# Kernel optimization log

Measured on AMD Instinct MI355X. Metric: run time of the kernel, lower is better.

The kernel has to match this reference:

```python
import jax, jax.numpy as jnp
import numpy as np

N_NODES = 8192
N_UND = 65536      # undirected pairs placed
N_DIR = 131072     # extra directed edges placed


def _build_graph():
    rng = np.random.default_rng(0)
    A = np.zeros((N_NODES, N_NODES), np.float32)
    # undirected pairs (i<j), both directions set
    ii = rng.integers(0, N_NODES, 4 * N_UND)
    jj = rng.integers(0, N_NODES, 4 * N_UND)
    m = ii < jj
    iu, ju = ii[m][:N_UND], jj[m][:N_UND]
    A[iu, ju] = 1.0
    A[ju, iu] = 1.0
    # extra directed edges
    di = rng.integers(0, N_NODES, 2 * N_DIR)
    dj = rng.integers(0, N_NODES, 2 * N_DIR)
    m2 = di != dj
    A[di[m2][:N_DIR], dj[m2][:N_DIR]] = 1.0
    # dense_to_sparse: row, col of nonzeros
    row, col = np.nonzero(A)
    edge_index = np.stack([row, col]).astype(np.int32)
    # undirected mask: A==1 & A.T==1, upper triangle
    und = np.triu((A == 1.0) & (A.T == 1.0))
    u, v = np.nonzero(und)
    undirected_edges = np.stack([u, v], axis=1).astype(np.int32)
    return A, edge_index, undirected_edges


def setup_inputs() -> dict:
    key = jax.random.key(0)
    ks = jax.random.split(key, 4)
    A, edge_index, undirected_edges = _build_graph()
    N = N_NODES
    return {
        "adjacency": jnp.asarray(A),
        "W1": jax.random.normal(ks[0], (N, 16), jnp.float32) * 0.05,
        "b1": jnp.zeros((16,), jnp.float32),
        "W2": jax.random.normal(ks[1], (16, 8), jnp.float32) * 0.25,
        "b2": jnp.zeros((8,), jnp.float32),
        "Wfc": jax.random.normal(ks[2], (16, 1), jnp.float32) * 0.25,
        "bfc": jnp.zeros((1,), jnp.float32),
        "edge_index": jnp.asarray(edge_index),
        "undirected_edges": jnp.asarray(undirected_edges),
    }


def reference(adjacency, W1, b1, W2, b2, Wfc, bfc, edge_index, undirected_edges):
    N = adjacency.shape[0]
    src, dst = edge_index[0], edge_index[1]
    E = src.shape[0]
    # GCN normalization with self-loops (PyG gcn_norm): deg over target nodes
    deg = jax.ops.segment_sum(jnp.ones((E,), adjacency.dtype), dst,
                              num_segments=N) + 1.0
    dinv = jax.lax.rsqrt(deg)                       # deg >= 1, no inf
    norm = dinv[src] * dinv[dst]                    # [E]
    self_w = (dinv * dinv)[:, None]                 # self-loop coeff [N,1]

    def conv(h):  # h: [N, F] -> normalized scatter-add aggregation
        msg = norm[:, None] * h[src]                # [E, F]
        return jax.ops.segment_sum(msg, dst, num_segments=N) + self_w * h

    # node_features = eye(N), so eye(N) @ W1 == W1
    x = jax.nn.relu(conv(W1) + b1)                  # [N, 16]
    x = jax.nn.relu(conv(x @ W2) + b2)              # [N, 8]

    u, v = undirected_edges[:, 0], undirected_edges[:, 1]
    ef = jnp.concatenate([x[u], x[v]], axis=1)      # [U, 16]
    orient = jax.nn.sigmoid(ef @ Wfc + bfc)[:, 0]   # [U]

    out = adjacency.at[u, v].set(orient).at[v, u].set(1.0 - orient)
    return out
```

## Files before the change

kernel.cpp:

```cpp
#include <hip/hip_runtime.h>
#include <math.h>

#define F1 16
#define F2 8

__global__ void k_edges0(const int* __restrict__ src, const int* __restrict__ dst,
                         float* __restrict__ out, float* __restrict__ deg,
                         int E, int N) {
    int e = blockIdx.x * blockDim.x + threadIdx.x;
    if (e < E) {
        int s = src[e], d = dst[e];
        out[(long)s * N + d] = 1.0f;
        atomicAdd(&deg[d], 1.0f);
    }
}

__global__ void k_conv1_edges(const int* __restrict__ src, const int* __restrict__ dst,
                              const float* __restrict__ deg, const float* __restrict__ W1,
                              float* __restrict__ x1, int E) {
    int id = blockIdx.x * blockDim.x + threadIdx.x;
    int e = id >> 4;
    int f = id & (F1 - 1);
    if (e < E) {
        int s = src[e], d = dst[e];
        float nrm = rsqrtf((deg[s] + 1.0f) * (deg[d] + 1.0f));
        atomicAdd(&x1[(long)d * F1 + f], nrm * W1[(long)s * F1 + f]);
    }
}

__global__ void k_layer1(const float* __restrict__ deg, const float* __restrict__ b1,
                         const float* __restrict__ W1, const float* __restrict__ W2,
                         const float* __restrict__ x1, float* __restrict__ h2, int N) {
    int id = blockIdx.x * blockDim.x + threadIdx.x;
    if (id < N * F2) {
        int i = id >> 3;
        int g = id & (F2 - 1);
        float sw = 1.0f / (deg[i] + 1.0f);
        float acc = 0.0f;
        #pragma unroll
        for (int f = 0; f < F1; ++f) {
            float v = x1[(long)i * F1 + f] + sw * W1[(long)i * F1 + f] + b1[f];
            v = v > 0.0f ? v : 0.0f;
            acc += v * W2[f * F2 + g];
        }
        h2[(long)i * F2 + g] = acc;
    }
}

__global__ void k_conv2_edges(const int* __restrict__ src, const int* __restrict__ dst,
                              const float* __restrict__ deg, const float* __restrict__ h2,
                              float* __restrict__ x2, int E) {
    int id = blockIdx.x * blockDim.x + threadIdx.x;
    int e = id >> 3;
    int g = id & (F2 - 1);
    if (e < E) {
        int s = src[e], d = dst[e];
        float nrm = rsqrtf((deg[s] + 1.0f) * (deg[d] + 1.0f));
        atomicAdd(&x2[(long)d * F2 + g], nrm * h2[(long)s * F2 + g]);
    }
}

__global__ void k_orient(const int2* __restrict__ ue, const float* __restrict__ x2,
                         const float* __restrict__ h2, const float* __restrict__ deg,
                         const float* __restrict__ b2, const float* __restrict__ Wfc,
                         const float* __restrict__ bfc, float* __restrict__ out,
                         int U, int N) {
    int k = blockIdx.x * blockDim.x + threadIdx.x;
    if (k < U) {
        int2 e = ue[k];
        int u = e.x, v = e.y;
        float swu = 1.0f / (deg[u] + 1.0f);
        float swv = 1.0f / (deg[v] + 1.0f);
        float s = bfc[0];
        #pragma unroll
        for (int g = 0; g < F2; ++g) {
            float xu = x2[(long)u * F2 + g] + swu * h2[(long)u * F2 + g] + b2[g];
            float xv = x2[(long)v * F2 + g] + swv * h2[(long)v * F2 + g] + b2[g];
            xu = xu > 0.0f ? xu : 0.0f;
            xv = xv > 0.0f ? xv : 0.0f;
            s += xu * Wfc[g] + xv * Wfc[F2 + g];
        }
        float orient = 1.0f / (1.0f + expf(-s));
        out[(long)u * N + v] = orient;
        out[(long)v * N + u] = 1.0f - orient;
    }
}

extern "C" void kernel_launch(void* const* d_in, const int* in_sizes, int n_in,
                              void* d_out, int out_size, void* d_ws, size_t ws_size,
                              hipStream_t stream) {
    const float* W1  = (const float*)d_in[1];
    const float* b1  = (const float*)d_in[2];
    const float* W2  = (const float*)d_in[3];
    const float* b2  = (const float*)d_in[4];
    const float* Wfc = (const float*)d_in[5];
    const float* bfc = (const float*)d_in[6];
    const int* edge_index = (const int*)d_in[7];
    const int2* und       = (const int2*)d_in[8];

    int N = in_sizes[1] / F1;
    int E = in_sizes[7] / 2;
    int U = in_sizes[8] / 2;
    const int* src = edge_index;
    const int* dst = edge_index + E;

    float* ws  = (float*)d_ws;
    float* deg = ws;
    float* x1  = ws + N;
    float* x2  = x1 + (long)F1 * N;
    float* h2  = x2 + (long)F2 * N;

    const int B = 256;

    hipMemsetAsync(d_out, 0, (size_t)N * N * sizeof(float), stream);
    hipMemsetAsync(d_ws, 0, (size_t)(N + (long)F1 * N + (long)F2 * N) * sizeof(float), stream);

    k_edges0<<<(E + B - 1) / B, B, 0, stream>>>(src, dst, (float*)d_out, deg, E, N);

    {
        long work = (long)E * F1;
        k_conv1_edges<<<(int)((work + B - 1) / B), B, 0, stream>>>(src, dst, deg, W1, x1, E);
    }
    k_layer1<<<(N * F2 + B - 1) / B, B, 0, stream>>>(deg, b1, W1, W2, x1, h2, N);

    {
        long work = (long)E * F2;
        k_conv2_edges<<<(int)((work + B - 1) / B), B, 0, stream>>>(src, dst, deg, h2, x2, E);
    }

    k_orient<<<(U + B - 1) / B, B, 0, stream>>>(und, x2, h2, deg, b2, Wfc, bfc,
                                                (float*)d_out, U, N);
}
```

Before: 448.6 us.

## Overlap output zero-fill with GCN stages and write edge ones last

The separate 256 MB memset of the dense output is removed. Its zeroing is split into three chunks, each handled by extra blocks added to the conv1, layer1 and conv2 kernels, so the bandwidth-bound fill runs alongside the small atomic-heavy graph kernels. Setting the 1.0 edge entries moves into the final orientation kernel, which now reads the input adjacency to skip reverse-present pairs, because those entries are overwritten by orientation values. This adds reads of the adjacency and makes the fill depend on the extra blocks being scheduled well.

```diff
diff --git a/kernel.cpp b/kernel.cpp
--- a/kernel.cpp
+++ b/kernel.cpp
@@ -4,67 +4,87 @@
 #define F1 16
 #define F2 8
 
-__global__ void k_edges0(const int* __restrict__ src, const int* __restrict__ dst,
-                         float* __restrict__ out, float* __restrict__ deg,
-                         int E, int N) {
+__global__ void k_deg(const int* __restrict__ dst, float* __restrict__ deg, int E) {
     int e = blockIdx.x * blockDim.x + threadIdx.x;
-    if (e < E) {
-        int s = src[e], d = dst[e];
-        out[(long)s * N + d] = 1.0f;
-        atomicAdd(&deg[d], 1.0f);
+    if (e < E) atomicAdd(&deg[dst[e]], 1.0f);
+}
+
+__global__ void k_conv1_fill(const int* __restrict__ src, const int* __restrict__ dst,
+                             const float* __restrict__ deg, const float* __restrict__ W1,
+                             float* __restrict__ x1, float4* __restrict__ out4,
+                             long f0, long f1, int E, int FB) {
+    if ((int)blockIdx.x < FB) {
+        const float4 z = make_float4(0.f, 0.f, 0.f, 0.f);
+        long stride = (long)FB * blockDim.x;
+        for (long i = f0 + (long)blockIdx.x * blockDim.x + threadIdx.x; i < f1; i += stride)
+            out4[i] = z;
+    } else {
+        long id = (long)(blockIdx.x - FB) * blockDim.x + threadIdx.x;
+        long e = id >> 4;
+        int f = (int)(id & (F1 - 1));
+        if (e < E) {
+            int s = src[e], d = dst[e];
+            float nrm = rsqrtf((deg[s] + 1.0f) * (deg[d] + 1.0f));
+            atomicAdd(&x1[(long)d * F1 + f], nrm * W1[(long)s * F1 + f]);
+        }
     }
 }
 
-__global__ void k_conv1_edges(const int* __restrict__ src, const int* __restrict__ dst,
-                              const float* __restrict__ deg, const float* __restrict__ W1,
-                              float* __restrict__ x1, int E) {
-    int id = blockIdx.x * blockDim.x + threadIdx.x;
-    int e = id >> 4;
-    int f = id & (F1 - 1);
-    if (e < E) {
-        int s = src[e], d = dst[e];
-        float nrm = rsqrtf((deg[s] + 1.0f) * (deg[d] + 1.0f));
-        atomicAdd(&x1[(long)d * F1 + f], nrm * W1[(long)s * F1 + f]);
+__global__ void k_layer1_fill(const float* __restrict__ deg, const float* __restrict__ b1,
+                              const float* __restrict__ W1, const float* __restrict__ W2,
+                              const float* __restrict__ x1, float* __restrict__ h2,
+                              float4* __restrict__ out4, long f0, long f1,
+                              int N, int FB) {
+    if ((int)blockIdx.x < FB) {
+        const float4 z = make_float4(0.f, 0.f, 0.f, 0.f);
+        long stride = (long)FB * blockDim.x;
+        for (long i = f0 + (long)blockIdx.x * blockDim.x + threadIdx.x; i < f1; i += stride)
+            out4[i] = z;
+    } else {
+        int id = (int)((blockIdx.x - FB) * blockDim.x + threadIdx.x);
+        if (id < N * F2) {
+            int i = id >> 3;
+            int g = id & (F2 - 1);
+            float sw = 1.0f / (deg[i] + 1.0f);
+            float acc = 0.0f;
+            #pragma unroll
+            for (int f = 0; f < F1; ++f) {
+                float v = x1[(long)i * F1 + f] + sw * W1[(long)i * F1 + f] + b1[f];
+                v = v > 0.0f ? v : 0.0f;
+                acc += v * W2[f * F2 + g];
+            }
+            h2[(long)i * F2 + g] = acc;
+        }
     }
 }
 
-__global__ void k_layer1(const float* __restrict__ deg, const float* __restrict__ b1,
-                         const float* __restrict__ W1, const float* __restrict__ W2,
-                         const float* __restrict__ x1, float* __restrict__ h2, int N) {
-    int id = blockIdx.x * blockDim.x + threadIdx.x;
-    if (id < N * F2) {
-        int i = id >> 3;
-        int g = id & (F2 - 1);
-        float sw = 1.0f / (deg[i] + 1.0f);
-        float acc = 0.0f;
-        #pragma unroll
-        for (int f = 0; f < F1; ++f) {
-            float v = x1[(long)i * F1 + f] + sw * W1[(long)i * F1 + f] + b1[f];
-            v = v > 0.0f ? v : 0.0f;
-            acc += v * W2[f * F2 + g];
+__global__ void k_conv2_fill(const int* __restrict__ src, const int* __restrict__ dst,
+                             const float* __restrict__ deg, const float* __restrict__ h2,
+                             float* __restrict__ x2, float4* __restrict__ out4,
+                             long f0, long f1, int E, int FB) {
+    if ((int)blockIdx.x < FB) {
+        const float4 z = make_float4(0.f, 0.f, 0.f, 0.f);
+        long stride = (long)FB * blockDim.x;
+        for (long i = f0 + (long)blockIdx.x * blockDim.x + threadIdx.x; i < f1; i += stride)
+            out4[i] = z;
+    } else {
+        long id = (long)(blockIdx.x - FB) * blockDim.x + threadIdx.x;
+        long e = id >> 3;
+        int g = (int)(id & (F2 - 1));
+        if (e < E) {
+            int s = src[e], d = dst[e];
+            float nrm = rsqrtf((deg[s] + 1.0f) * (deg[d] + 1.0f));
+            atomicAdd(&x2[(long)d * F2 + g], nrm * h2[(long)s * F2 + g]);
         }
-        h2[(long)i * F2 + g] = acc;
     }
 }
 
-__global__ void k_conv2_edges(const int* __restrict__ src, const int* __restrict__ dst,
-                              const float* __restrict__ deg, const float* __restrict__ h2,
-                              float* __restrict__ x2, int E) {
-    int id = blockIdx.x * blockDim.x + threadIdx.x;
-    int e = id >> 3;
-    int g = id & (F2 - 1);
-    if (e < E) {
-        int s = src[e], d = dst[e];
-        float nrm = rsqrtf((deg[s] + 1.0f) * (deg[d] + 1.0f));
-        atomicAdd(&x2[(long)d * F2 + g], nrm * h2[(long)s * F2 + g]);
-    }
-}
-
-__global__ void k_orient(const int2* __restrict__ ue, const float* __restrict__ x2,
-                         const float* __restrict__ h2, const float* __restrict__ deg,
-                         const float* __restrict__ b2, const float* __restrict__ Wfc,
-                         const float* __restrict__ bfc, float* __restrict__ out,
-                         int U, int N) {
+__global__ void k_orient_ones(const int2* __restrict__ ue, const int* __restrict__ src,
+                              const int* __restrict__ dst, const float* __restrict__ adj,
+                              const float* __restrict__ x2, const float* __restrict__ h2,
+                              const float* __restrict__ deg, const float* __restrict__ b2,
+                              const float* __restrict__ Wfc, const float* __restrict__ bfc,
+                              float* __restrict__ out, int U, int E, int N) {
     int k = blockIdx.x * blockDim.x + threadIdx.x;
     if (k < U) {
         int2 e = ue[k];
@@ -83,12 +103,18 @@
         float orient = 1.0f / (1.0f + expf(-s));
         out[(long)u * N + v] = orient;
         out[(long)v * N + u] = 1.0f - orient;
+    } else if (k < U + E) {
+        int e = k - U;
+        int s = src[e], d = dst[e];
+        if (adj[(long)d * N + s] == 0.0f)
+            out[(long)s * N + d] = 1.0f;
     }
 }
 
 extern "C" void kernel_launch(void* const* d_in, const int* in_sizes, int n_in,
                               void* d_out, int out_size, void* d_ws, size_t ws_size,
                               hipStream_t stream) {
+    const float* adj = (const float*)d_in[0];
     const float* W1  = (const float*)d_in[1];
     const float* b1  = (const float*)d_in[2];
     const float* W2  = (const float*)d_in[3];
@@ -110,24 +136,30 @@
     float* x2  = x1 + (long)F1 * N;
     float* h2  = x2 + (long)F2 * N;
 
+    float4* out4 = (float4*)d_out;
+    const long Z4 = (long)N * N / 4;
+    const long c1 = Z4 / 3, c2 = Z4 * 2 / 3;
+
     const int B = 256;
+    const int FB = 2048;
 
-    hipMemsetAsync(d_out, 0, (size_t)N * N * sizeof(float), stream);
     hipMemsetAsync(d_ws, 0, (size_t)(N + (long)F1 * N + (long)F2 * N) * sizeof(float), stream);
 
-    k_edges0<<<(E + B - 1) / B, B, 0, stream>>>(src, dst, (float*)d_out, deg, E, N);
+    k_deg<<<(E + B - 1) / B, B, 0, stream>>>(dst, deg, E);
 
     {
-        long work = (long)E * F1;
-        k_conv1_edges<<<(int)((work + B - 1) / B), B, 0, stream>>>(src, dst, deg, W1, x1, E);
+        int cb = (int)(((long)E * F1 + B - 1) / B);
+        k_conv1_fill<<<FB + cb, B, 0, stream>>>(src, dst, deg, W1, x1, out4, 0, c1, E, FB);
     }
-    k_layer1<<<(N * F2 + B - 1) / B, B, 0, stream>>>(deg, b1, W1, W2, x1, h2, N);
-
     {
-        long work = (long)E * F2;
-        k_conv2_edges<<<(int)((work + B - 1) / B), B, 0, stream>>>(src, dst, deg, h2, x2, E);
+        int cb = (N * F2 + B - 1) / B;
+        k_layer1_fill<<<FB + cb, B, 0, stream>>>(deg, b1, W1, W2, x1, h2, out4, c1, c2, N, FB);
     }
-
-    k_orient<<<(U + B - 1) / B, B, 0, stream>>>(und, x2, h2, deg, b2, Wfc, bfc,
-                                                (float*)d_out, U, N);
+    {
+        int cb = (int)(((long)E * F2 + B - 1) / B);
+        k_conv2_fill<<<FB + cb, B, 0, stream>>>(src, dst, deg, h2, x2, out4, c2, Z4, E, FB);
+    }
+    k_orient_ones<<<(U + E + B - 1) / B, B, 0, stream>>>(und, src, dst, adj, x2, h2, deg,
+                                                         b2, Wfc, bfc, (float*)d_out,
+                                                         U, E, N);
 }
```

Result: slower. 477.9 us (+6.5%).
